# Kernel optimization log

Hardware: AMD Instinct MI355X
Metric: run time of the kernel (lower is better)

## Reference

```python
import jax, jax.numpy as jnp
import numpy as np


def _mlp(x, W1, b1, W2, b2):
    # x: (B, M, T); torch MLPLayer: transpose(1,2) -> Linear -> Linear -> LeakyReLU -> transpose back
    h = jnp.einsum('bmt,hm->bht', x, W1) + b1[None, :, None]   # (B, H, T)
    y = jnp.einsum('bht,oh->bot', h, W2) + b2[None, :, None]   # (B, M, T)
    return jax.nn.leaky_relu(y, negative_slope=0.01)


def _calc_attn(q, k, v):
    # q: (B, M, Tq), k: (B, M, Tk), v: (B, M, Tk)
    Tq = q.shape[-1]
    qk = jnp.einsum('bmq,bmk->bqk', q, k)                       # (B, Tq, Tk)
    eye = jnp.eye(Tq, dtype=qk.dtype)                           # broadcasts: (Tq,Tq) or (1,1)
    logits = jnp.exp(qk - qk * eye / jnp.sqrt(jnp.asarray(Tq, qk.dtype)))
    scores = jax.nn.softmax(logits, axis=-1)
    return jnp.einsum('bqk,bmk->bmq', scores, v)                # (B, M, Tq)


def setup_inputs() -> dict:
    key = jax.random.key(0)
    B, M, T, H = 16, 128, 2048, 512
    ks = jax.random.split(key, 14)
    s = 0.02
    inp = {
        'pattern': jax.random.normal(ks[0], (B, M, T), jnp.float32),
        'value': jax.random.normal(ks[1], (B, M, T), jnp.float32),
        'kernel_size': 33,
    }
    names = ['q', 'k', 'o']
    for i, n in enumerate(names):
        inp['W%s1' % n] = jax.random.normal(ks[2 + 4 * i], (H, M), jnp.float32) * s
        inp['b%s1' % n] = jax.random.normal(ks[3 + 4 * i], (H,), jnp.float32) * s
        inp['W%s2' % n] = jax.random.normal(ks[4 + 4 * i], (M, H), jnp.float32) * s
        inp['b%s2' % n] = jax.random.normal(ks[5 + 4 * i], (M,), jnp.float32) * s
    return inp


def reference(pattern, value, kernel_size, Wq1, bq1, Wq2, bq2, Wk1, bk1, Wk2, bk2, Wo1, bo1, Wo2, bo2):
    query = _mlp(pattern, Wq1, bq1, Wq2, bq2)
    key = _mlp(pattern, Wk1, bk1, Wk2, bk2)
    # full (internal) attention
    attn_in = _calc_attn(query, key, value)                     # (B, M, T)
    rep_in = _mlp(attn_in, Wo1, bo1, Wo2, bo2)
    # windowed (external) attention
    T = query.shape[-1]
    cu = (kernel_size - 1) // 2
    q_w = query[..., T - 1 - cu : T - cu]                       # (B, M, 1)
    k_w = key[..., kernel_size - cu - 1 : T - cu - 2]           # (B, M, T-k-1)
    v_w = value[..., kernel_size : T - 1]                       # (B, M, T-k-1)
    attn_ex = _calc_attn(q_w, k_w, v_w)                         # (B, M, 1)
    rep_ex = _mlp(attn_ex, Wo1, bo1, Wo2, bo2)
    return jnp.concatenate([rep_in, rep_ex], axis=-1)           # (B, M, T+1)
```

## Files before the change

kernel.cpp:

```cpp
#include <hip/hip_runtime.h>
#include <hip/hip_bf16.h>
#include <math.h>

#define B_    16
#define M_    128
#define T_    2048
#define H_    512
#define TOUT_ 2049

typedef unsigned short u16;
typedef unsigned int   u32;
typedef __bf16 bf16x8 __attribute__((ext_vector_type(8)));
typedef float  f32x16 __attribute__((ext_vector_type(16)));
typedef u32    u32x4  __attribute__((ext_vector_type(4)));
typedef u32    u32x2  __attribute__((ext_vector_type(2)));

#define A_OFF     0
#define C_OFF     16384
#define MEAN_OFF  16896
#define AQKBF_OFF 19200
#define AOBF_OFF  35584
#define QT_OFF    43776
#define KT_OFF    (43776 + 2097152)
#define VB_OFF    (43776 + 2 * 2097152)

static __device__ __forceinline__ u16 f2bf(float f) {
  u32 u = __float_as_uint(f);
  u = (u + 0x7FFFu + ((u >> 16) & 1u)) >> 16;
  return (u16)u;
}
static __device__ __forceinline__ u32 pk2(float lo, float hi) {
  __hip_bfloat162 h = __float22bfloat162_rn(float2{lo, hi});
  u32 r;
  __builtin_memcpy(&r, &h, 4);
  return r;
}
static __device__ __forceinline__ bf16x8 ldfrag(const u16* p) {
  return __builtin_bit_cast(bf16x8, *(const u32x4*)p);
}

__global__ __launch_bounds__(128) void fuse_weights_all(
    const float* __restrict__ W1q, const float* __restrict__ b1q,
    const float* __restrict__ W2q, const float* __restrict__ b2q,
    const float* __restrict__ W1k, const float* __restrict__ b1k,
    const float* __restrict__ W2k, const float* __restrict__ b2k,
    const float* __restrict__ W1o, const float* __restrict__ b1o,
    const float* __restrict__ W2o, const float* __restrict__ b2o,
    float* __restrict__ A, float* __restrict__ c,
    u16* __restrict__ Aqk_bf, u16* __restrict__ Ao_bf) {
  __shared__ float w2row[H_];
  int which = blockIdx.x >> 7;
  int o = blockIdx.x & 127;
  const float* W1 = which == 0 ? W1q : which == 1 ? W1k : W1o;
  const float* b1 = which == 0 ? b1q : which == 1 ? b1k : b1o;
  const float* W2 = which == 0 ? W2q : which == 1 ? W2k : W2o;
  const float* b2 = which == 0 ? b2q : which == 1 ? b2k : b2o;
  int m = threadIdx.x;
  for (int h = m; h < H_; h += 128) w2row[h] = W2[o * H_ + h];
  __syncthreads();
  float acc = 0.f;
#pragma unroll 8
  for (int h = 0; h < H_; ++h) acc = fmaf(w2row[h], W1[h * M_ + m], acc);
  u16 ab = f2bf(acc);
  if (which == 0)      Aqk_bf[o * 128 + m] = ab;
  else if (which == 1) Aqk_bf[(128 + o) * 128 + m] = ab;
  else               { Ao_bf[o * 128 + m] = ab; A[o * M_ + m] = acc; }
  if (m < 64) {
    float cc = 0.f;
    for (int h = m; h < H_; h += 64) cc = fmaf(w2row[h], b1[h], cc);
#pragma unroll
    for (int off = 32; off > 0; off >>= 1) cc += __shfl_down(cc, off, 64);
    if (m == 0) c[which * 128 + o] = cc + b2[o];
  }
}

#define XS 68

__global__ __launch_bounds__(256) void prep_kernel(
    const float* __restrict__ pattern, const u16* __restrict__ Aqk_bf,
    const float* __restrict__ cqk, u16* __restrict__ qT, u16* __restrict__ kT,
    const float* __restrict__ value, u16* __restrict__ vb,
    float* __restrict__ meanv) {
  __shared__ alignas(16) float xsf[128 * XS];
  int bx = blockIdx.x;
  int tid = threadIdx.x;

  if (bx >= 512) {
    int bm = bx - 512;
    float* red = xsf;
    const float* row = value + (size_t)bm * T_;
    int i0 = tid * 8;
    float4 a = *(const float4*)(row + i0);
    float4 bq = *(const float4*)(row + i0 + 4);
    u32x4 o = {pk2(a.x, a.y), pk2(a.z, a.w), pk2(bq.x, bq.y), pk2(bq.z, bq.w)};
    *(u32x4*)&vb[(size_t)bm * T_ + i0] = o;
    float vals[8] = {a.x, a.y, a.z, a.w, bq.x, bq.y, bq.z, bq.w};
    float s = 0.f;
#pragma unroll
    for (int j = 0; j < 8; ++j) {
      int idx = i0 + j;
      if (idx >= 33 && idx < T_ - 1) s += vals[j];
    }
    red[tid] = s;
    __syncthreads();
    for (int st = 128; st > 0; st >>= 1) {
      if (tid < st) red[tid] += red[tid + st];
      __syncthreads();
    }
    if (tid == 0) meanv[bm] = red[0] * (1.f / 2014.f);
    return;
  }

  int b = bx >> 5;
  int t0 = (bx & 31) * 64;
  int lane = tid & 63;
  int wv = tid >> 6;
  int l31 = lane & 31;
  int lh8 = (lane >> 5) * 8;

  bf16x8 afr[2][8];
#pragma unroll
  for (int i = 0; i < 2; ++i) {
    const u16* ap = Aqk_bf + ((2 * wv + i) * 32 + l31) * 128 + lh8;
#pragma unroll
    for (int s = 0; s < 8; ++s) afr[i][s] = ldfrag(ap + 16 * s);
  }

#pragma unroll
  for (int rep = 0; rep < 8; ++rep) {
    int m = rep * 16 + (tid >> 4);
    int tc = (tid & 15) * 4;
    float4 v = *(const float4*)&pattern[(size_t)(b * M_ + m) * T_ + t0 + tc];
    *(float4*)&xsf[m * XS + tc] = v;
  }
  __syncthreads();

  bf16x8 bfr[2][8];
#pragma unroll
  for (int tt = 0; tt < 2; ++tt) {
#pragma unroll
    for (int s = 0; s < 8; ++s) {
      float v0 = xsf[(s * 16 + lh8 + 0) * XS + tt * 32 + l31];
      float v1 = xsf[(s * 16 + lh8 + 1) * XS + tt * 32 + l31];
      float v2 = xsf[(s * 16 + lh8 + 2) * XS + tt * 32 + l31];
      float v3 = xsf[(s * 16 + lh8 + 3) * XS + tt * 32 + l31];
      float v4 = xsf[(s * 16 + lh8 + 4) * XS + tt * 32 + l31];
      float v5 = xsf[(s * 16 + lh8 + 5) * XS + tt * 32 + l31];
      float v6 = xsf[(s * 16 + lh8 + 6) * XS + tt * 32 + l31];
      float v7 = xsf[(s * 16 + lh8 + 7) * XS + tt * 32 + l31];
      u32x4 p = {pk2(v0, v1), pk2(v2, v3), pk2(v4, v5), pk2(v6, v7)};
      bfr[tt][s] = __builtin_bit_cast(bf16x8, p);
    }
  }
  __syncthreads();

  u16* obuf = (u16*)xsf;
#pragma unroll
  for (int tt = 0; tt < 2; ++tt) {
#pragma unroll
    for (int i = 0; i < 2; ++i) {
      f32x16 acc;
#pragma unroll
      for (int r = 0; r < 16; ++r) acc[r] = 0.f;
#pragma unroll
      for (int s = 0; s < 8; ++s)
        acc = __builtin_amdgcn_mfma_f32_32x32x16_bf16(afr[i][s], bfr[tt][s], acc, 0, 0, 0);
      int ot = 2 * wv + i;
      int t = tt * 32 + l31;
#pragma unroll
      for (int r = 0; r < 16; ++r) {
        int orow = (r & 3) + 8 * (r >> 2) + 4 * (lane >> 5);
        float v = acc[r] + cqk[ot * 32 + orow];
        v = v > 0.f ? v : 0.01f * v;
        obuf[t * 258 + ot * 32 + orow] = f2bf(v);
      }
    }
  }
  __syncthreads();

  const u32* ob32 = (const u32*)obuf;
#pragma unroll
  for (int g = 0; g < 8; ++g) {
    int G = wv * 8 + g;
    int mat = G >> 4;
    int t = (G & 15) * 4 + (lane >> 4);
    int og2 = lane & 15;
    int wbase = t * 129 + mat * 64 + og2 * 4;
    u32x4 vv = {ob32[wbase], ob32[wbase + 1], ob32[wbase + 2], ob32[wbase + 3]};
    u32* dst = (u32*)((mat ? kT : qT) + ((size_t)(b * T_ + t0 + t)) * 128) + og2 * 4;
    *(u32x4*)dst = vv;
  }
}

#define QSTR 136
#define VSTR 72
#define NKT  (T_ / 64)

__global__ __launch_bounds__(512, 2) void attn_mfma_kernel(
    const u16* __restrict__ qT, const u16* __restrict__ kT,
    const u16* __restrict__ vB, const u16* __restrict__ Ao_bf,
    const float* __restrict__ co, const float* __restrict__ Aofp,
    const float* __restrict__ meanv, float* __restrict__ out) {
  extern __shared__ u16 smem[];
  u16* qsw = smem;
  u16* ks  = smem + 128 * QSTR;
  u16* vs0 = ks + 64 * QSTR;
  u16* vs1 = vs0 + 128 * VSTR;
  float* dls = (float*)(vs1 + 128 * VSTR);

  int b = blockIdx.y;
  int q0 = blockIdx.x * 128;
  int tid = threadIdx.x;
  int lane = tid & 63;
  int wv = tid >> 6;
  int l31 = lane & 31;
  int lh8 = (lane >> 5) * 8;

  {
    const u16* gq = qT + (size_t)(b * T_ + q0) * 128;
#pragma unroll
    for (int it = 0; it < 4; ++it) {
      int r = it * 32 + (tid >> 4);
      int cm = (tid & 15) * 8;
      *(u32x4*)&qsw[r * QSTR + cm] = *(const u32x4*)&gq[r * 128 + cm];
    }
  }

  const u16* gkb = kT + (size_t)b * T_ * 128;
  const u16* gvb = vB + (size_t)b * M_ * T_;
  int kr = tid >> 4, kc = (tid & 15) * 8;
  int vr = tid >> 3, vc = (tid & 7) * 8;

  u32x4 kreg[2], vreg[2];
#pragma unroll
  for (int it = 0; it < 2; ++it) {
    kreg[it] = *(const u32x4*)&gkb[(size_t)(it * 32 + kr) * 128 + kc];
    vreg[it] = *(const u32x4*)&gvb[(size_t)(it * 64 + vr) * T_ + vc];
  }

  __syncthreads();

  int qw = (wv & 3) * 32;
  int kw = (wv >> 2) * 32;
  bf16x8 afrag[8];
  {
    const u16* qrow = &qsw[(qw + l31) * QSTR + lh8];
#pragma unroll
    for (int s = 0; s < 8; ++s) afrag[s] = ldfrag(qrow + s * 16);
  }

  int qt = wv & 3;
  int mb = (wv >> 2) * 2;

#pragma unroll
  for (int it = 0; it < 2; ++it) {
    *(u32x4*)&ks[(it * 32 + kr) * QSTR + kc] = kreg[it];
    *(u32x4*)&vs0[(it * 64 + vr) * VSTR + vc] = vreg[it];
  }
#pragma unroll
  for (int it = 0; it < 2; ++it) {
    kreg[it] = *(const u32x4*)&gkb[(size_t)(64 + it * 32 + kr) * 128 + kc];
    vreg[it] = *(const u32x4*)&gvb[(size_t)(it * 64 + vr) * T_ + 64 + vc];
  }

  f32x16 pacc[2];
  float dreg[16];
#pragma unroll
  for (int i = 0; i < 16; ++i) { pacc[0][i] = 0.f; pacc[1][i] = 0.f; dreg[i] = 0.f; }

  for (int kt = 0; kt < NKT; ++kt) {
    int k0 = kt * 64;
    u16* vcur = (kt & 1) ? vs1 : vs0;
    u16* vnxt = (kt & 1) ? vs0 : vs1;
    __syncthreads();

    f32x16 sacc;
#pragma unroll
    for (int i = 0; i < 16; ++i) sacc[i] = 0.f;
    {
      const u16* krow = &ks[(kw + l31) * QSTR + lh8];
#pragma unroll
      for (int s = 0; s < 8; ++s) {
        bf16x8 bf = ldfrag(krow + s * 16);
        sacc = __builtin_amdgcn_mfma_f32_32x32x16_bf16(afrag[s], bf, sacc, 0, 0, 0);
      }
    }

    int kl = kw + l31;
    if (q0 + qw == k0 + kw) {
#pragma unroll
      for (int r = 0; r < 16; ++r) {
        int qrow = qw + (r & 3) + 8 * (r >> 2) + 4 * (lane >> 5);
        if (qrow == kl + (k0 - q0)) sacc[r] *= 0.97790291f;
      }
    }
#pragma unroll
    for (int r = 0; r < 16; r += 2) {
      int qrow = qw + (r & 3) + 8 * (r >> 2) + 4 * (lane >> 5);
      float w0 = __expf(__expf(sacc[r]));
      float w1 = __expf(__expf(sacc[r + 1]));
      u32 p = pk2(w0, w1);
      dreg[r]     += __uint_as_float(p << 16);
      dreg[r + 1] += __uint_as_float(p & 0xffff0000u);
      qsw[qrow * VSTR + kl]       = (u16)p;
      qsw[(qrow + 1) * VSTR + kl] = (u16)(p >> 16);
    }
    __syncthreads();

    if (kt < NKT - 1) {
#pragma unroll
      for (int it = 0; it < 2; ++it) {
        *(u32x4*)&ks[(it * 32 + kr) * QSTR + kc] = kreg[it];
        *(u32x4*)&vnxt[(it * 64 + vr) * VSTR + vc] = vreg[it];
      }
      int kn = (kt + 2 < NKT) ? (kt + 2) * 64 : (NKT - 1) * 64;
#pragma unroll
      for (int it = 0; it < 2; ++it) {
        kreg[it] = *(const u32x4*)&gkb[(size_t)(kn + it * 32 + kr) * 128 + kc];
        vreg[it] = *(const u32x4*)&gvb[(size_t)(it * 64 + vr) * T_ + kn + vc];
      }
    }

#pragma unroll
    for (int s2 = 0; s2 < 4; ++s2) {
      bf16x8 wf = ldfrag(&qsw[(qt * 32 + l31) * VSTR + s2 * 16 + lh8]);
      bf16x8 vf0 = ldfrag(&vcur[(mb * 32 + l31) * VSTR + s2 * 16 + lh8]);
      bf16x8 vf1 = ldfrag(&vcur[((mb + 1) * 32 + l31) * VSTR + s2 * 16 + lh8]);
      pacc[0] = __builtin_amdgcn_mfma_f32_32x32x16_bf16(vf0, wf, pacc[0], 0, 0, 0);
      pacc[1] = __builtin_amdgcn_mfma_f32_32x32x16_bf16(vf1, wf, pacc[1], 0, 0, 0);
    }
  }

#pragma unroll
  for (int r = 0; r < 16; ++r) {
    float d = dreg[r];
    for (int off = 1; off < 32; off <<= 1) d += __shfl_xor(d, off, 64);
    dreg[r] = d;
  }
  if (l31 == 0) {
#pragma unroll
    for (int r = 0; r < 16; ++r) {
      int qrow = qw + (r & 3) + 8 * (r >> 2) + 4 * (lane >> 5);
      dls[(wv >> 2) * 128 + qrow] = dreg[r];
    }
  }
  __syncthreads();

  {
    int qcol = qt * 32 + l31;
    float rden = 1.f / (dls[qcol] + dls[128 + qcol]);
#pragma unroll
    for (int mi = 0; mi < 2; ++mi) {
      int mbase = (mb + mi) * 32 + 4 * (lane >> 5);
#pragma unroll
      for (int g = 0; g < 4; ++g) {
        float v0 = pacc[mi][4 * g + 0] * rden;
        float v1 = pacc[mi][4 * g + 1] * rden;
        float v2 = pacc[mi][4 * g + 2] * rden;
        float v3 = pacc[mi][4 * g + 3] * rden;
        u32x2 w = {pk2(v0, v1), pk2(v2, v3)};
        *(u32x2*)&qsw[qcol * QSTR + mbase + 8 * g] = w;
      }
    }
  }
  __syncthreads();

  bf16x8 aofr[8];
  {
    const u16* ap = Ao_bf + ((wv & 3) * 32 + l31) * 128 + lh8;
#pragma unroll
    for (int s = 0; s < 8; ++s) aofr[s] = ldfrag(ap + 16 * s);
  }
#pragma unroll
  for (int j = 0; j < 2; ++j) {
    int qt2 = (wv >> 2) * 2 + j;
    bf16x8 pfr[8];
    const u16* pp = &qsw[(qt2 * 32 + l31) * QSTR + lh8];
#pragma unroll
    for (int s = 0; s < 8; ++s) pfr[s] = ldfrag(pp + 16 * s);
    f32x16 oacc;
#pragma unroll
    for (int r = 0; r < 16; ++r) oacc[r] = 0.f;
#pragma unroll
    for (int s = 0; s < 8; ++s)
      oacc = __builtin_amdgcn_mfma_f32_32x32x16_bf16(aofr[s], pfr[s], oacc, 0, 0, 0);
#pragma unroll
    for (int r = 0; r < 16; ++r) {
      int orow = (wv & 3) * 32 + (r & 3) + 8 * (r >> 2) + 4 * (lane >> 5);
      float v = oacc[r] + co[orow];
      v = v > 0.f ? v : 0.01f * v;
      out[((size_t)(b * M_ + orow)) * TOUT_ + q0 + qt2 * 32 + l31] = v;
    }
  }

  if (blockIdx.x == 0 && tid < 128) {
    float acc = co[tid];
    const float* mv = meanv + b * 128;
    for (int m = 0; m < 128; ++m) acc = fmaf(Aofp[tid * 128 + m], mv[m], acc);
    acc = acc > 0.f ? acc : 0.01f * acc;
    out[((size_t)(b * M_ + tid)) * TOUT_ + 2048] = acc;
  }
}

extern "C" void kernel_launch(void* const* d_in, const int* in_sizes, int n_in,
                              void* d_out, int out_size, void* d_ws, size_t ws_size,
                              hipStream_t stream) {
  (void)in_sizes; (void)n_in; (void)out_size; (void)ws_size;
  const float* pattern = (const float*)d_in[0];
  const float* value   = (const float*)d_in[1];
  const float* Wq1 = (const float*)d_in[3];
  const float* bq1 = (const float*)d_in[4];
  const float* Wq2 = (const float*)d_in[5];
  const float* bq2 = (const float*)d_in[6];
  const float* Wk1 = (const float*)d_in[7];
  const float* bk1 = (const float*)d_in[8];
  const float* Wk2 = (const float*)d_in[9];
  const float* bk2 = (const float*)d_in[10];
  const float* Wo1 = (const float*)d_in[11];
  const float* bo1 = (const float*)d_in[12];
  const float* Wo2 = (const float*)d_in[13];
  const float* bo2 = (const float*)d_in[14];

  float* ws     = (float*)d_ws;
  float* A      = ws + A_OFF;
  float* c      = ws + C_OFF;
  float* meanv  = ws + MEAN_OFF;
  u16*   Aqk_bf = (u16*)(ws + AQKBF_OFF);
  u16*   Ao_bf  = (u16*)(ws + AOBF_OFF);
  u16*   qT     = (u16*)(ws + QT_OFF);
  u16*   kT     = (u16*)(ws + KT_OFF);
  u16*   vB     = (u16*)(ws + VB_OFF);
  float* out    = (float*)d_out;

  fuse_weights_all<<<384, 128, 0, stream>>>(
      Wq1, bq1, Wq2, bq2, Wk1, bk1, Wk2, bk2, Wo1, bo1, Wo2, bo2,
      A, c, Aqk_bf, Ao_bf);

  prep_kernel<<<512 + B_ * M_, 256, 0, stream>>>(
      pattern, Aqk_bf, c, qT, kT, value, vB, meanv);

  size_t lds_bytes = (128 * QSTR + 64 * QSTR + 2 * 128 * VSTR) * sizeof(u16)
                   + 256 * sizeof(float);
  attn_mfma_kernel<<<dim3(T_ / 128, B_), 512, lds_bytes, stream>>>(
      qT, kT, vB, Ao_bf, c + 256, A, meanv, out);
}
```

Measured before the change: 192.8 us.

## Keep attention weights in registers and double-buffer K tiles

The QK^T MFMA is transposed so that each wave's score tile lands in the register layout the PV MFMA expects as its B operand. Weights are packed to bf16 and exchanged across half-waves with shuffles instead of going through LDS. K gets a second LDS buffer, which removes one barrier per key tile. The two key-half waves now each accumulate all 128 value rows over their half of the keys and are reduced through LDS at the end. The cost is twice as many accumulator registers (four f32x16 tiles), which may hurt occupancy under the 512x2 launch bounds, plus extra LDS for the second K buffer.

```diff
diff --git a/kernel.cpp b/kernel.cpp
--- a/kernel.cpp
+++ b/kernel.cpp
@@ -12,6 +12,7 @@
 typedef unsigned int   u32;
 typedef __bf16 bf16x8 __attribute__((ext_vector_type(8)));
 typedef float  f32x16 __attribute__((ext_vector_type(16)));
+typedef float  f32x4  __attribute__((ext_vector_type(4)));
 typedef u32    u32x4  __attribute__((ext_vector_type(4)));
 typedef u32    u32x2  __attribute__((ext_vector_type(2)));
 
@@ -203,10 +204,12 @@
     const float* __restrict__ meanv, float* __restrict__ out) {
   extern __shared__ u16 smem[];
   u16* qsw = smem;
-  u16* ks  = smem + 128 * QSTR;
-  u16* vs0 = ks + 64 * QSTR;
+  u16* ks0 = smem + 128 * QSTR;
+  u16* ks1 = ks0 + 64 * QSTR;
+  u16* vs0 = ks1 + 64 * QSTR;
   u16* vs1 = vs0 + 128 * VSTR;
-  float* dls = (float*)(vs1 + 128 * VSTR);
+  float* dls  = (float*)(vs1 + 128 * VSTR);
+  float* pbuf = (float*)ks0;
 
   int b = blockIdx.y;
   int q0 = blockIdx.x * 128;
@@ -214,7 +217,10 @@
   int lane = tid & 63;
   int wv = tid >> 6;
   int l31 = lane & 31;
-  int lh8 = (lane >> 5) * 8;
+  int h = lane >> 5;
+  int lh8 = h * 8;
+  int qt = wv & 3;
+  int kh = wv >> 2;
 
   {
     const u16* gq = qT + (size_t)(b * T_ + q0) * 128;
@@ -240,21 +246,16 @@
 
   __syncthreads();
 
-  int qw = (wv & 3) * 32;
-  int kw = (wv >> 2) * 32;
-  bf16x8 afrag[8];
+  bf16x8 qfrag[8];
   {
-    const u16* qrow = &qsw[(qw + l31) * QSTR + lh8];
-#pragma unroll
-    for (int s = 0; s < 8; ++s) afrag[s] = ldfrag(qrow + s * 16);
-  }
-
-  int qt = wv & 3;
-  int mb = (wv >> 2) * 2;
+    const u16* qrow = &qsw[(qt * 32 + l31) * QSTR + lh8];
+#pragma unroll
+    for (int s = 0; s < 8; ++s) qfrag[s] = ldfrag(qrow + s * 16);
+  }
 
 #pragma unroll
   for (int it = 0; it < 2; ++it) {
-    *(u32x4*)&ks[(it * 32 + kr) * QSTR + kc] = kreg[it];
+    *(u32x4*)&ks0[(it * 32 + kr) * QSTR + kc] = kreg[it];
     *(u32x4*)&vs0[(it * 64 + vr) * VSTR + vc] = vreg[it];
   }
 #pragma unroll
@@ -263,54 +264,25 @@
     vreg[it] = *(const u32x4*)&gvb[(size_t)(it * 64 + vr) * T_ + 64 + vc];
   }
 
-  f32x16 pacc[2];
-  float dreg[16];
-#pragma unroll
-  for (int i = 0; i < 16; ++i) { pacc[0][i] = 0.f; pacc[1][i] = 0.f; dreg[i] = 0.f; }
+  f32x16 pacc[4];
+  float den = 0.f;
+#pragma unroll
+  for (int i = 0; i < 16; ++i) {
+    pacc[0][i] = 0.f; pacc[1][i] = 0.f; pacc[2][i] = 0.f; pacc[3][i] = 0.f;
+  }
 
   for (int kt = 0; kt < NKT; ++kt) {
     int k0 = kt * 64;
+    u16* kcur = (kt & 1) ? ks1 : ks0;
+    u16* knxt = (kt & 1) ? ks0 : ks1;
     u16* vcur = (kt & 1) ? vs1 : vs0;
     u16* vnxt = (kt & 1) ? vs0 : vs1;
     __syncthreads();
 
-    f32x16 sacc;
-#pragma unroll
-    for (int i = 0; i < 16; ++i) sacc[i] = 0.f;
-    {
-      const u16* krow = &ks[(kw + l31) * QSTR + lh8];
-#pragma unroll
-      for (int s = 0; s < 8; ++s) {
-        bf16x8 bf = ldfrag(krow + s * 16);
-        sacc = __builtin_amdgcn_mfma_f32_32x32x16_bf16(afrag[s], bf, sacc, 0, 0, 0);
-      }
-    }
-
-    int kl = kw + l31;
-    if (q0 + qw == k0 + kw) {
-#pragma unroll
-      for (int r = 0; r < 16; ++r) {
-        int qrow = qw + (r & 3) + 8 * (r >> 2) + 4 * (lane >> 5);
-        if (qrow == kl + (k0 - q0)) sacc[r] *= 0.97790291f;
-      }
-    }
-#pragma unroll
-    for (int r = 0; r < 16; r += 2) {
-      int qrow = qw + (r & 3) + 8 * (r >> 2) + 4 * (lane >> 5);
-      float w0 = __expf(__expf(sacc[r]));
-      float w1 = __expf(__expf(sacc[r + 1]));
-      u32 p = pk2(w0, w1);
-      dreg[r]     += __uint_as_float(p << 16);
-      dreg[r + 1] += __uint_as_float(p & 0xffff0000u);
-      qsw[qrow * VSTR + kl]       = (u16)p;
-      qsw[(qrow + 1) * VSTR + kl] = (u16)(p >> 16);
-    }
-    __syncthreads();
-
     if (kt < NKT - 1) {
 #pragma unroll
       for (int it = 0; it < 2; ++it) {
-        *(u32x4*)&ks[(it * 32 + kr) * QSTR + kc] = kreg[it];
+        *(u32x4*)&knxt[(it * 32 + kr) * QSTR + kc] = kreg[it];
         *(u32x4*)&vnxt[(it * 64 + vr) * VSTR + vc] = vreg[it];
       }
       int kn = (kt + 2 < NKT) ? (kt + 2) * 64 : (NKT - 1) * 64;
@@ -321,45 +293,88 @@
       }
     }
 
-#pragma unroll
-    for (int s2 = 0; s2 < 4; ++s2) {
-      bf16x8 wf = ldfrag(&qsw[(qt * 32 + l31) * VSTR + s2 * 16 + lh8]);
-      bf16x8 vf0 = ldfrag(&vcur[(mb * 32 + l31) * VSTR + s2 * 16 + lh8]);
-      bf16x8 vf1 = ldfrag(&vcur[((mb + 1) * 32 + l31) * VSTR + s2 * 16 + lh8]);
-      pacc[0] = __builtin_amdgcn_mfma_f32_32x32x16_bf16(vf0, wf, pacc[0], 0, 0, 0);
-      pacc[1] = __builtin_amdgcn_mfma_f32_32x32x16_bf16(vf1, wf, pacc[1], 0, 0, 0);
-    }
-  }
-
-#pragma unroll
-  for (int r = 0; r < 16; ++r) {
-    float d = dreg[r];
-    for (int off = 1; off < 32; off <<= 1) d += __shfl_xor(d, off, 64);
-    dreg[r] = d;
-  }
-  if (l31 == 0) {
-#pragma unroll
-    for (int r = 0; r < 16; ++r) {
-      int qrow = qw + (r & 3) + 8 * (r >> 2) + 4 * (lane >> 5);
-      dls[(wv >> 2) * 128 + qrow] = dreg[r];
-    }
-  }
-  __syncthreads();
-
-  {
-    int qcol = qt * 32 + l31;
-    float rden = 1.f / (dls[qcol] + dls[128 + qcol]);
-#pragma unroll
-    for (int mi = 0; mi < 2; ++mi) {
-      int mbase = (mb + mi) * 32 + 4 * (lane >> 5);
+    f32x16 sacc;
+#pragma unroll
+    for (int i = 0; i < 16; ++i) sacc[i] = 0.f;
+    {
+      const u16* krow = &kcur[(kh * 32 + l31) * QSTR + lh8];
+#pragma unroll
+      for (int s = 0; s < 8; ++s) {
+        bf16x8 kf = ldfrag(krow + s * 16);
+        sacc = __builtin_amdgcn_mfma_f32_32x32x16_bf16(kf, qfrag[s], sacc, 0, 0, 0);
+      }
+    }
+
+    if (k0 + kh * 32 == q0 + qt * 32) {
+#pragma unroll
+      for (int r = 0; r < 16; ++r) {
+        int row = (r & 3) + 8 * (r >> 2) + 4 * h;
+        if (row == l31) sacc[r] *= 0.97790291f;
+      }
+    }
+
+    float w[16];
+#pragma unroll
+    for (int r = 0; r < 16; ++r) w[r] = __expf(__expf(sacc[r]));
+#pragma unroll
+    for (int r = 0; r < 16; ++r) den += w[r];
+    u32 p00 = pk2(w[0], w[1]),  p01 = pk2(w[2], w[3]);
+    u32 p10 = pk2(w[4], w[5]),  p11 = pk2(w[6], w[7]);
+    u32 p20 = pk2(w[8], w[9]),  p21 = pk2(w[10], w[11]);
+    u32 p30 = pk2(w[12], w[13]), p31 = pk2(w[14], w[15]);
+    u32 e0 = __shfl_xor(h ? p00 : p10, 32, 64);
+    u32 e1 = __shfl_xor(h ? p01 : p11, 32, 64);
+    u32 e2 = __shfl_xor(h ? p20 : p30, 32, 64);
+    u32 e3 = __shfl_xor(h ? p21 : p31, 32, 64);
+    u32x4 f0 = h ? u32x4{e0, e1, p10, p11} : u32x4{p00, p01, e0, e1};
+    u32x4 f1 = h ? u32x4{e2, e3, p30, p31} : u32x4{p20, p21, e2, e3};
+    bf16x8 bw0 = __builtin_bit_cast(bf16x8, f0);
+    bf16x8 bw1 = __builtin_bit_cast(bf16x8, f1);
+
+#pragma unroll
+    for (int mt = 0; mt < 4; ++mt) {
+      const u16* vrow = &vcur[(mt * 32 + l31) * VSTR + kh * 32 + lh8];
+      bf16x8 vf0 = ldfrag(vrow);
+      bf16x8 vf1 = ldfrag(vrow + 16);
+      pacc[mt] = __builtin_amdgcn_mfma_f32_32x32x16_bf16(vf0, bw0, pacc[mt], 0, 0, 0);
+      pacc[mt] = __builtin_amdgcn_mfma_f32_32x32x16_bf16(vf1, bw1, pacc[mt], 0, 0, 0);
+    }
+  }
+
+  float dq = den + __shfl_xor(den, 32, 64);
+
+  __syncthreads();
+
+  if (kh == 1) {
+#pragma unroll
+    for (int mt = 0; mt < 4; ++mt) {
+      float* pb = &pbuf[((size_t)(qt * 4 + mt) * 64 + lane) * 16];
 #pragma unroll
       for (int g = 0; g < 4; ++g) {
-        float v0 = pacc[mi][4 * g + 0] * rden;
-        float v1 = pacc[mi][4 * g + 1] * rden;
-        float v2 = pacc[mi][4 * g + 2] * rden;
-        float v3 = pacc[mi][4 * g + 3] * rden;
-        u32x2 w = {pk2(v0, v1), pk2(v2, v3)};
-        *(u32x2*)&qsw[qcol * QSTR + mbase + 8 * g] = w;
+        f32x4 v = {pacc[mt][4 * g], pacc[mt][4 * g + 1],
+                   pacc[mt][4 * g + 2], pacc[mt][4 * g + 3]};
+        *(f32x4*)(pb + 4 * g) = v;
+      }
+    }
+    if (lane < 32) dls[qt * 32 + lane] = dq;
+  }
+  __syncthreads();
+
+  if (kh == 0) {
+    float rden = 1.f / (dq + dls[qt * 32 + l31]);
+#pragma unroll
+    for (int mt = 0; mt < 4; ++mt) {
+      const float* pb = &pbuf[((size_t)(qt * 4 + mt) * 64 + lane) * 16];
+#pragma unroll
+      for (int g = 0; g < 4; ++g) {
+        f32x4 t = *(const f32x4*)(pb + 4 * g);
+        float v0 = (pacc[mt][4 * g + 0] + t[0]) * rden;
+        float v1 = (pacc[mt][4 * g + 1] + t[1]) * rden;
+        float v2 = (pacc[mt][4 * g + 2] + t[2]) * rden;
+        float v3 = (pacc[mt][4 * g + 3] + t[3]) * rden;
+        int m0 = mt * 32 + 8 * g + 4 * h;
+        u32x2 wp = {pk2(v0, v1), pk2(v2, v3)};
+        *(u32x2*)&qsw[(qt * 32 + l31) * QSTR + m0] = wp;
       }
     }
   }
@@ -373,7 +388,7 @@
   }
 #pragma unroll
   for (int j = 0; j < 2; ++j) {
-    int qt2 = (wv >> 2) * 2 + j;
+    int qt2 = kh * 2 + j;
     bf16x8 pfr[8];
     const u16* pp = &qsw[(qt2 * 32 + l31) * QSTR + lh8];
 #pragma unroll
@@ -386,7 +401,7 @@
       oacc = __builtin_amdgcn_mfma_f32_32x32x16_bf16(aofr[s], pfr[s], oacc, 0, 0, 0);
 #pragma unroll
     for (int r = 0; r < 16; ++r) {
-      int orow = (wv & 3) * 32 + (r & 3) + 8 * (r >> 2) + 4 * (lane >> 5);
+      int orow = (wv & 3) * 32 + (r & 3) + 8 * (r >> 2) + 4 * h;
       float v = oacc[r] + co[orow];
       v = v > 0.f ? v : 0.01f * v;
       out[((size_t)(b * M_ + orow)) * TOUT_ + q0 + qt2 * 32 + l31] = v;
@@ -439,8 +454,8 @@
   prep_kernel<<<512 + B_ * M_, 256, 0, stream>>>(
       pattern, Aqk_bf, c, qT, kT, value, vB, meanv);
 
-  size_t lds_bytes = (128 * QSTR + 64 * QSTR + 2 * 128 * VSTR) * sizeof(u16)
-                   + 256 * sizeof(float);
+  size_t lds_bytes = (size_t)(128 * QSTR + 2 * 64 * QSTR + 2 * 128 * VSTR) * 2
+                   + 128 * 4;
   attn_mfma_kernel<<<dim3(T_ / 128, B_), 512, lds_bytes, stream>>>(
       qT, kT, vB, Ao_bf, c + 256, A, meanv, out);
 }
```

Measured after the change: 193.0 us (median of 2 runs). Within noise of the previous version (+0.1%).
